# Kernel tuning notes

Measured on AMD Instinct MI355X. Metric: run time of the kernel, lower is better.

Reference implementation:

```python
import jax, jax.numpy as jnp
import numpy as np

K, MU, SIGMA = 8, 0.0, 0.1
M, N, D_DIM, T = 512, 1024, 512, 4096


def setup_inputs() -> dict:
    key = jax.random.key(0)
    ks, ke, ka, kd, kl1, kl2 = jax.random.split(key, 6)
    S = jax.random.normal(ks, (N, T), dtype=jnp.float32)
    E = jax.random.normal(ke, (M, T), dtype=jnp.float32)  # raw noise; scaled by sigma/mu in reference
    A = jax.random.uniform(ka, (M, N), dtype=jnp.float32)  # torch.rand init
    Dm = jax.random.normal(kd, (N, D_DIM), dtype=jnp.float32) / jnp.sqrt(N)  # stands in for DCT-transformed randn
    c = jnp.ones((1,), dtype=jnp.float32)
    l1 = 0.1 * jnp.abs(jax.random.normal(kl1, (1,), dtype=jnp.float32)) + 0.05
    l2 = jax.random.normal(kl2, (1,), dtype=jnp.float32)
    # LISTA params per layer; all K layers get the same closed-form init in the original
    U1 = jnp.eye(D_DIM, dtype=jnp.float32) - (1.0 / c[0]) * (Dm.T @ A.T @ A @ Dm)  # [d,d]
    V1 = (1.0 / c[0]) * (Dm.T @ A.T)  # [d,m]
    U = jnp.broadcast_to(U1, (K, D_DIM, D_DIM)).copy()
    V = jnp.broadcast_to(V1, (K, D_DIM, M)).copy()
    H0 = jnp.zeros((D_DIM, T), dtype=jnp.float32)
    return {"S": S, "E": E, "A": A, "D": Dm, "U": U, "V": V, "l1": l1, "l2": l2, "c": c, "H0": H0}


def reference(S, E, A, D, U, V, l1, l2, c, H0):
    # X = A @ S + noise (E ~ randn, scaled as in torch forward)
    X = A @ S + (E * SIGMA + MU)  # [m,T]
    # Self-attention on H0 (the original loop always feeds self.H, the zero buffer,
    # into every layer -- H is never chained). Attention map = softmax((D@H0)^T (D@H0)).
    G = D @ H0                                   # [n,T]
    attn = jax.nn.softmax(G.T @ G, axis=-1)      # [T,T]
    Z = l2[0] * (H0 @ attn)                      # [d,T]
    # All K LISTA updates share the same (H0-derived) Z and X -> batch over layers.
    mat = jnp.einsum('kde,et->kdt', U, Z) + jnp.einsum('kdm,mt->kdt', V, X)  # [K,d,T]
    thres = l1[0] / c[0]
    H_all = jnp.sign(mat) * jnp.maximum(jnp.zeros((), mat.dtype), jnp.abs(mat) - thres)
    H_last = H_all[-1]                           # only the last layer's H survives the loop
    return D @ H_last                            # S_star [n,T]
```

## Files before the change

kernel.cpp:

```cpp
#include <hip/hip_runtime.h>

typedef unsigned short ushort_t;
typedef unsigned int u32;
typedef ushort_t u16x8 __attribute__((ext_vector_type(8)));
typedef ushort_t u16x4 __attribute__((ext_vector_type(4)));
typedef __bf16   bf16x8 __attribute__((ext_vector_type(8)));
typedef float    f32x4  __attribute__((ext_vector_type(4)));

#define T_DIM 4096

__device__ __forceinline__ ushort_t f2bf(float f){
  union { float f; unsigned u; } x; x.f = f;
  unsigned r = x.u + 0x7FFFu + ((x.u >> 16) & 1u);
  return (ushort_t)(r >> 16);
}

__device__ __forceinline__ void gload16(const void* g, void* l){
  __builtin_amdgcn_global_load_lds(
      (const __attribute__((address_space(1))) u32*)g,
      (__attribute__((address_space(3))) u32*)l, 16, 0, 0);
}

__global__ __launch_bounds__(256) void prep_kernel(
    const float* __restrict__ S, const float* __restrict__ A,
    const float* __restrict__ V7, const float* __restrict__ Dm,
    ushort_t* __restrict__ St, ushort_t* __restrict__ Abf,
    ushort_t* __restrict__ Vbf, ushort_t* __restrict__ Dbf)
{
  __shared__ float tile[64][65];
  const int bid = blockIdx.x, tid = threadIdx.x;
  if (bid < 1024){
    const int t0 = (bid & 63) * 64, n0 = (bid >> 6) * 64;
#pragma unroll
    for (int i = 0; i < 4; ++i){
      int g = tid + 256 * i; int row = g >> 4, cq = g & 15;
      const f32x4 v = *(const f32x4*)&S[(size_t)(n0 + row) * T_DIM + t0 + cq * 4];
#pragma unroll
      for (int j = 0; j < 4; ++j) tile[row][cq * 4 + j] = v[j];
    }
    __syncthreads();
#pragma unroll
    for (int i = 0; i < 2; ++i){
      int g = tid + 256 * i; int tl = g >> 3, nq = g & 7;
      u16x8 h;
#pragma unroll
      for (int j = 0; j < 8; ++j) h[j] = f2bf(tile[nq * 8 + j][tl]);
      *(u16x8*)&St[(size_t)(t0 + tl) * 1024 + n0 + ((nq ^ (tl & 7)) << 3)] = h;
    }
  } else {
    int pid = bid - 1024;
    const float* src; ushort_t* dst; int g, ks;
    if (pid < 256)      { src = A;  dst = Abf; g = pid * 256 + tid;        ks = 7; }
    else if (pid < 384) { src = V7; dst = Vbf; g = (pid - 256) * 256 + tid; ks = 6; }
    else                { src = Dm; dst = Dbf; g = (pid - 384) * 256 + tid; ks = 6; }
    const int r = g >> ks, cg = g & ((1 << ks) - 1);
    const int Kd = 8 << ks;
    const size_t base = (size_t)r * Kd + (size_t)cg * 8;
    const f32x4 v0 = *(const f32x4*)&src[base];
    const f32x4 v1 = *(const f32x4*)&src[base + 4];
    u16x8 h;
#pragma unroll
    for (int j = 0; j < 4; ++j){ h[j] = f2bf(v0[j]); h[j + 4] = f2bf(v1[j]); }
    *(u16x8*)&dst[(size_t)r * Kd + ((cg >> 3) << 6) + ((((cg & 7) ^ (r & 7))) << 3)] = h;
  }
}

template<int EPI, int BM>
__global__ __launch_bounds__(256) void gemm_kernel(
    const ushort_t* __restrict__ Ag, const ushort_t* __restrict__ Bg,
    void* __restrict__ Cout, const float* __restrict__ Eptr,
    const float* __restrict__ l1p, const float* __restrict__ cp,
    const int Kd)
{
  constexpr int MF = BM / 32;
  constexpr bool SWAP = (EPI != 2);
  __shared__ __align__(16) ushort_t As[2][BM * 64];
  __shared__ __align__(16) ushort_t Bs[2][64 * 64];
  const int tid = threadIdx.x;
  const int lane = tid & 63, wid = tid >> 6;
  const int wm = wid >> 1, wn = wid & 1;
  const int lr = lane & 15, lq = lane >> 4;
  const int t0 = blockIdx.x * BM, n0 = blockIdx.y * 64;

  constexpr int P = SWAP ? 2 : MF;
  constexpr int Q = SWAP ? MF : 2;
  f32x4 acc[P][Q];
#pragma unroll
  for (int i = 0; i < P; ++i)
#pragma unroll
    for (int j = 0; j < Q; ++j) acc[i][j] = (f32x4){0.f, 0.f, 0.f, 0.f};

  auto stage = [&](int kt, int b){
#pragma unroll
    for (int i = 0; i < BM / 32; ++i){
      int c = i * 256 + tid;
      gload16(&Ag[(size_t)(t0 + (c >> 3)) * Kd + kt * 64 + (c & 7) * 8],
              &As[b][(i * 256 + (tid & 192)) * 8]);
    }
#pragma unroll
    for (int i = 0; i < 2; ++i){
      int c = i * 256 + tid;
      gload16(&Bg[(size_t)(n0 + (c >> 3)) * Kd + kt * 64 + (c & 7) * 8],
              &Bs[b][(i * 256 + (tid & 192)) * 8]);
    }
  };

  auto compute = [&](int b){
#pragma unroll
    for (int ksv = 0; ksv < 2; ++ksv){
      const int kb = ksv * 4 + lq;
      bf16x8 a[MF], bb[2];
#pragma unroll
      for (int mf = 0; mf < MF; ++mf){
        int r = wm * (BM / 2) + mf * 16 + lr;
        a[mf] = *(const bf16x8*)&As[b][r * 64 + ((kb ^ (r & 7)) << 3)];
      }
#pragma unroll
      for (int nf = 0; nf < 2; ++nf){
        int r = wn * 32 + nf * 16 + lr;
        bb[nf] = *(const bf16x8*)&Bs[b][r * 64 + ((kb ^ (r & 7)) << 3)];
      }
      if constexpr (SWAP){
#pragma unroll
        for (int nf = 0; nf < 2; ++nf)
#pragma unroll
          for (int mf = 0; mf < MF; ++mf)
            acc[nf][mf] = __builtin_amdgcn_mfma_f32_16x16x32_bf16(
                bb[nf], a[mf], acc[nf][mf], 0, 0, 0);
      } else {
#pragma unroll
        for (int mf = 0; mf < MF; ++mf)
#pragma unroll
          for (int nf = 0; nf < 2; ++nf)
            acc[mf][nf] = __builtin_amdgcn_mfma_f32_16x16x32_bf16(
                a[mf], bb[nf], acc[mf][nf], 0, 0, 0);
      }
    }
  };

  const int nk = Kd >> 6;
  stage(0, 0);
  for (int kt = 0; kt < nk; ++kt){
    __syncthreads();
    if (kt + 1 < nk) stage(kt + 1, (kt + 1) & 1);
    compute(kt & 1);
  }

  if constexpr (EPI == 2){
    float* O = (float*)Cout;
#pragma unroll
    for (int mf = 0; mf < MF; ++mf)
#pragma unroll
      for (int nf = 0; nf < 2; ++nf){
        const int t = t0 + wm * (BM / 2) + mf * 16 + lq * 4;
        const int n = n0 + wn * 32 + nf * 16 + lr;
        *(f32x4*)&O[(size_t)n * T_DIM + t] = acc[mf][nf];
      }
  } else {
    const float thres = (EPI == 1) ? (l1p[0] / cp[0]) : 0.f;
    ushort_t* OT = (ushort_t*)Cout;
#pragma unroll
    for (int nf = 0; nf < 2; ++nf){
#pragma unroll
      for (int mf = 0; mf < MF; ++mf){
        const int m = n0 + wn * 32 + nf * 16 + lq * 4;
        const int t = t0 + wm * (BM / 2) + mf * 16 + lr;
        f32x4 v = acc[nf][mf];
        u16x4 h;
        if constexpr (EPI == 0){
#pragma unroll
          for (int j = 0; j < 4; ++j){
            float e = Eptr[(size_t)(m + j) * T_DIM + t];
            h[j] = f2bf(v[j] + 0.1f * e);
          }
        } else {
#pragma unroll
          for (int j = 0; j < 4; ++j){
            float av = fabsf(v[j]) - thres;
            float r = av > 0.f ? (v[j] > 0.f ? av : -av) : 0.f;
            h[j] = f2bf(r);
          }
        }
        *(u16x4*)&OT[(size_t)t * 512 + (m & ~63) +
                     (((((m >> 3) & 7) ^ (t & 7))) << 3) + (m & 7)] = h;
      }
    }
  }
}

extern "C" void kernel_launch(void* const* d_in, const int* in_sizes, int n_in,
                              void* d_out, int out_size, void* d_ws, size_t ws_size,
                              hipStream_t stream)
{
  const float* S  = (const float*)d_in[0];
  const float* E  = (const float*)d_in[1];
  const float* A  = (const float*)d_in[2];
  const float* Dm = (const float*)d_in[3];
  const float* V  = (const float*)d_in[5];
  const float* l1 = (const float*)d_in[6];
  const float* c  = (const float*)d_in[8];

  char* ws = (char*)d_ws;
  ushort_t* St  = (ushort_t*)(ws);
  ushort_t* XT  = (ushort_t*)(ws + (size_t)( 8u << 20));
  ushort_t* HT  = (ushort_t*)(ws + (size_t)(12u << 20));
  ushort_t* Abf = (ushort_t*)(ws + (size_t)(16u << 20));
  ushort_t* Vbf = (ushort_t*)(ws + (size_t)(17u << 20));
  ushort_t* Dbf = (ushort_t*)(ws + (size_t)(17u << 20) + (512u << 10));
  const float* V7 = V + (size_t)7 * 512 * 512;

  prep_kernel<<<1664, 256, 0, stream>>>(S, A, V7, Dm, St, Abf, Vbf, Dbf);
  gemm_kernel<0, 64><<<dim3(64, 8), 256, 0, stream>>>(St, Abf, (void*)XT, E, nullptr, nullptr, 1024);
  gemm_kernel<1, 64><<<dim3(64, 8), 256, 0, stream>>>(XT, Vbf, (void*)HT, nullptr, l1, c, 512);
  gemm_kernel<2, 128><<<dim3(32, 16), 256, 0, stream>>>(HT, Dbf, d_out, nullptr, nullptr, nullptr, 512);
}
```

Measured before the change: 43.43 us.

## Triple-buffer GEMM k-loop with explicit vmcnt waits and 128-row tiles

```diff
diff --git a/kernel.cpp b/kernel.cpp
--- a/kernel.cpp
+++ b/kernel.cpp
@@ -65,22 +65,22 @@
   }
 }
 
-template<int EPI, int BM>
+template<int EPI, int KD>
 __global__ __launch_bounds__(256) void gemm_kernel(
     const ushort_t* __restrict__ Ag, const ushort_t* __restrict__ Bg,
     void* __restrict__ Cout, const float* __restrict__ Eptr,
-    const float* __restrict__ l1p, const float* __restrict__ cp,
-    const int Kd)
+    const float* __restrict__ l1p, const float* __restrict__ cp)
 {
-  constexpr int MF = BM / 32;
+  constexpr int NK = KD / 64;
   constexpr bool SWAP = (EPI != 2);
-  __shared__ __align__(16) ushort_t As[2][BM * 64];
-  __shared__ __align__(16) ushort_t Bs[2][64 * 64];
+  constexpr int MF = 4;
+  __shared__ __align__(16) ushort_t As[3][128 * 64];
+  __shared__ __align__(16) ushort_t Bs[3][64 * 64];
   const int tid = threadIdx.x;
   const int lane = tid & 63, wid = tid >> 6;
   const int wm = wid >> 1, wn = wid & 1;
   const int lr = lane & 15, lq = lane >> 4;
-  const int t0 = blockIdx.x * BM, n0 = blockIdx.y * 64;
+  const int t0 = blockIdx.x * 128, n0 = blockIdx.y * 64;
 
   constexpr int P = SWAP ? 2 : MF;
   constexpr int Q = SWAP ? MF : 2;
@@ -92,15 +92,15 @@
 
   auto stage = [&](int kt, int b){
 #pragma unroll
-    for (int i = 0; i < BM / 32; ++i){
+    for (int i = 0; i < 4; ++i){
       int c = i * 256 + tid;
-      gload16(&Ag[(size_t)(t0 + (c >> 3)) * Kd + kt * 64 + (c & 7) * 8],
+      gload16(&Ag[(size_t)(t0 + (c >> 3)) * KD + kt * 64 + (c & 7) * 8],
               &As[b][(i * 256 + (tid & 192)) * 8]);
     }
 #pragma unroll
     for (int i = 0; i < 2; ++i){
       int c = i * 256 + tid;
-      gload16(&Bg[(size_t)(n0 + (c >> 3)) * Kd + kt * 64 + (c & 7) * 8],
+      gload16(&Bg[(size_t)(n0 + (c >> 3)) * KD + kt * 64 + (c & 7) * 8],
               &Bs[b][(i * 256 + (tid & 192)) * 8]);
     }
   };
@@ -112,7 +112,7 @@
       bf16x8 a[MF], bb[2];
 #pragma unroll
       for (int mf = 0; mf < MF; ++mf){
-        int r = wm * (BM / 2) + mf * 16 + lr;
+        int r = wm * 64 + mf * 16 + lr;
         a[mf] = *(const bf16x8*)&As[b][r * 64 + ((kb ^ (r & 7)) << 3)];
       }
 #pragma unroll
@@ -138,12 +138,15 @@
     }
   };
 
-  const int nk = Kd >> 6;
   stage(0, 0);
-  for (int kt = 0; kt < nk; ++kt){
-    __syncthreads();
-    if (kt + 1 < nk) stage(kt + 1, (kt + 1) & 1);
-    compute(kt & 1);
+  stage(1, 1);
+  for (int kt = 0; kt < NK; ++kt){
+    if (kt < NK - 1) { asm volatile("s_waitcnt vmcnt(6)" ::: "memory"); }
+    else             { asm volatile("s_waitcnt vmcnt(0)" ::: "memory"); }
+    __builtin_amdgcn_s_barrier();
+    __builtin_amdgcn_sched_barrier(0);
+    if (kt + 2 < NK) stage(kt + 2, (kt + 2) % 3);
+    compute(kt % 3);
   }
 
   if constexpr (EPI == 2){
@@ -152,7 +155,7 @@
     for (int mf = 0; mf < MF; ++mf)
 #pragma unroll
       for (int nf = 0; nf < 2; ++nf){
-        const int t = t0 + wm * (BM / 2) + mf * 16 + lq * 4;
+        const int t = t0 + wm * 64 + mf * 16 + lq * 4;
         const int n = n0 + wn * 32 + nf * 16 + lr;
         *(f32x4*)&O[(size_t)n * T_DIM + t] = acc[mf][nf];
       }
@@ -164,7 +167,7 @@
 #pragma unroll
       for (int mf = 0; mf < MF; ++mf){
         const int m = n0 + wn * 32 + nf * 16 + lq * 4;
-        const int t = t0 + wm * (BM / 2) + mf * 16 + lr;
+        const int t = t0 + wm * 64 + mf * 16 + lr;
         f32x4 v = acc[nf][mf];
         u16x4 h;
         if constexpr (EPI == 0){
@@ -210,7 +213,7 @@
   const float* V7 = V + (size_t)7 * 512 * 512;
 
   prep_kernel<<<1664, 256, 0, stream>>>(S, A, V7, Dm, St, Abf, Vbf, Dbf);
-  gemm_kernel<0, 64><<<dim3(64, 8), 256, 0, stream>>>(St, Abf, (void*)XT, E, nullptr, nullptr, 1024);
-  gemm_kernel<1, 64><<<dim3(64, 8), 256, 0, stream>>>(XT, Vbf, (void*)HT, nullptr, l1, c, 512);
-  gemm_kernel<2, 128><<<dim3(32, 16), 256, 0, stream>>>(HT, Dbf, d_out, nullptr, nullptr, nullptr, 512);
-}
+  gemm_kernel<0, 1024><<<dim3(32, 8), 256, 0, stream>>>(St, Abf, (void*)XT, E, nullptr, nullptr);
+  gemm_kernel<1, 512><<<dim3(32, 8), 256, 0, stream>>>(XT, Vbf, (void*)HT, nullptr, l1, c);
+  gemm_kernel<2, 512><<<dim3(32, 16), 256, 0, stream>>>(HT, Dbf, d_out, nullptr, nullptr, nullptr);
+}
```

Measured after the change: 43.93 us. About the same (+1.1%).
